# Optimization experiments

Hardware: AMD Instinct MI355X
Metric: run time of the kernel (lower is better)

## Reference

```python
import jax, jax.numpy as jnp
import numpy as np

BS = 16
CIN = 32          # input_channels
COUT = 64         # out_channels
OUT_DIM = 1024    # out_dim
S = 2
S0 = 1
K = S * (S0 + 1)  # non-overlapping patch size = 4
D = OUT_DIM * K   # input spatial length = 4096


def setup_inputs() -> dict:
    key = jax.random.key(0)
    k1, k2 = jax.random.split(key)
    x = jax.random.normal(k1, (BS, CIN, D), dtype=jnp.float32)
    # learned parameter, torch.randn init
    weight = jax.random.normal(k2, (COUT, CIN, D), dtype=jnp.float32)
    return {"x": x, "weight": weight}


def reference(x, weight):
    # sharing == 0 path of NonOverlappingLocallyConnected1d:
    #   out[b,o,p] = (1/sqrt(CIN)) * sum_{c,k} x[b,c,p*K+k] * weight[o,c,p*K+k]
    # Original materializes [bs,cout,cin,D] via broadcast multiply then sums
    # over (cin, K); fused here as a single einsum over non-overlapping patches.
    bs = x.shape[0]
    xr = x.reshape(bs, CIN, OUT_DIM, K)        # [b, c, p, k]
    wr = weight.reshape(COUT, CIN, OUT_DIM, K)  # [o, c, p, k]
    out = jnp.einsum('bcpk,ocpk->bop', xr, wr)  # [b, o, p]
    return out / jnp.sqrt(jnp.asarray(CIN, x.dtype))
```

## Files before the change

### kernel.cpp

```cpp
#include <hip/hip_runtime.h>

#define BS      16
#define CIN     32
#define COUT    64
#define OUT_DIM 1024
#define RS4     1024

__global__ __launch_bounds__(256, 6) void nolc1d_kernel(
    const float* __restrict__ x,
    const float* __restrict__ w,
    float* __restrict__ out)
{
    const int bid = blockIdx.x;
    const int xcd = bid & 7;
    const int j   = bid >> 3;
    const int og  = j & 15;
    const int bs  = (j >> 4) & 3;
    const int pg  = xcd + 8 * (j >> 6);
    const int o0  = og * 4;
    const int b0  = bs * 4;
    const int pf0 = pg * 32;

    const int t    = threadIdx.x;
    const int lane = t & 63;
    const int wv   = t >> 6;
    const int cs   = t >> 5;
    const int pp   = t & 31;

    const float4* __restrict__ x4 = (const float4*)x;
    const float4* __restrict__ w4 = (const float4*)w;

    float acc[4][4] = {};

    #pragma unroll 1
    for (int k = 0; k < 4; ++k) {
        const int c = cs + 8 * k;
        float4 xv[4];
        #pragma unroll
        for (int bi = 0; bi < 4; ++bi)
            xv[bi] = x4[((b0 + bi) * CIN + c) * RS4 + pf0 + pp];
        #pragma unroll
        for (int o = 0; o < 4; ++o) {
            const float4 wq = w4[((o0 + o) * CIN + c) * RS4 + pf0 + pp];
            #pragma unroll
            for (int bi = 0; bi < 4; ++bi)
                acc[bi][o] += xv[bi].x * wq.x + xv[bi].y * wq.y +
                              xv[bi].z * wq.z + xv[bi].w * wq.w;
        }
    }

    #pragma unroll
    for (int bi = 0; bi < 4; ++bi)
        #pragma unroll
        for (int o = 0; o < 4; ++o)
            acc[bi][o] += __shfl_xor(acc[bi][o], 32, 64);

    __shared__ float red[4][4][4][32];
    if (lane < 32) {
        #pragma unroll
        for (int bi = 0; bi < 4; ++bi)
            #pragma unroll
            for (int o = 0; o < 4; ++o)
                red[wv][bi][o][pp] = acc[bi][o];
    }
    __syncthreads();

    const float scale = 0.17677669529663687f;
    #pragma unroll
    for (int rep = 0; rep < 2; ++rep) {
        const int idx = t + 256 * rep;
        const int b   = idx >> 7;
        const int o   = (idx >> 5) & 3;
        const int p2  = idx & 31;
        const float s = red[0][b][o][p2] + red[1][b][o][p2] +
                        red[2][b][o][p2] + red[3][b][o][p2];
        out[((size_t)(b0 + b) * COUT + o0 + o) * OUT_DIM + pg * 32 + p2] =
            s * scale;
    }
}

extern "C" void kernel_launch(void* const* d_in, const int* in_sizes, int n_in,
                              void* d_out, int out_size, void* d_ws, size_t ws_size,
                              hipStream_t stream) {
    const float* x = (const float*)d_in[0];
    const float* w = (const float*)d_in[1];
    float* out = (float*)d_out;

    nolc1d_kernel<<<dim3(2048), dim3(256), 0, stream>>>(x, w, out);
}
```

Baseline: 87.12 us.

## Stage weight tile in LDS via direct global-to-LDS loads and cover all batches per block

Each block now handles all 16 batches for a 4-output, 32-patch tile, using 1024 threads instead of 256. The block's weight slice is loaded once into shared memory with global_load_lds, so weights are no longer refetched once per batch group across blocks. The cross-channel reduction reuses the same LDS buffer. In exchange, blocks are larger with 64KB LDS, the grid is smaller, and the weight load is not overlapped with compute, which may lower occupancy and latency hiding.

```diff
diff --git a/kernel.cpp b/kernel.cpp
--- a/kernel.cpp
+++ b/kernel.cpp
@@ -6,7 +6,7 @@
 #define OUT_DIM 1024
 #define RS4     1024
 
-__global__ __launch_bounds__(256, 6) void nolc1d_kernel(
+__global__ __launch_bounds__(1024, 8) void nolc1d_kernel(
     const float* __restrict__ x,
     const float* __restrict__ w,
     float* __restrict__ out)
@@ -15,37 +15,62 @@
     const int xcd = bid & 7;
     const int j   = bid >> 3;
     const int og  = j & 15;
-    const int bs  = (j >> 4) & 3;
-    const int pg  = xcd + 8 * (j >> 6);
+    const int pg  = xcd + 8 * (j >> 4);
     const int o0  = og * 4;
-    const int b0  = bs * 4;
     const int pf0 = pg * 32;
 
     const int t    = threadIdx.x;
     const int lane = t & 63;
     const int wv   = t >> 6;
-    const int cs   = t >> 5;
+    const int g    = t >> 8;
+    const int cs   = (t >> 5) & 7;
     const int pp   = t & 31;
+
+    __shared__ float4 ws[4096];
 
     const float4* __restrict__ x4 = (const float4*)x;
     const float4* __restrict__ w4 = (const float4*)w;
 
+    {
+        const int half = lane >> 5;
+        const int q    = lane & 31;
+        #pragma unroll
+        for (int i = 0; i < 4; ++i) {
+            const int s   = wv * 4 + i;
+            const int row = 2 * s + half;
+            const int cc  = row >> 2;
+            const int oo  = row & 3;
+            const float4* src =
+                &w4[((o0 + oo) * CIN + cc) * RS4 + pf0 + q];
+            float4* dst = &ws[s * 64];
+            __builtin_amdgcn_global_load_lds(
+                (const __attribute__((address_space(1))) void*)src,
+                (__attribute__((address_space(3))) void*)dst,
+                16, 0, 0);
+        }
+    }
+    __syncthreads();
+
     float acc[4][4] = {};
-
     #pragma unroll 1
     for (int k = 0; k < 4; ++k) {
-        const int c = cs + 8 * k;
-        float4 xv[4];
-        #pragma unroll
-        for (int bi = 0; bi < 4; ++bi)
-            xv[bi] = x4[((b0 + bi) * CIN + c) * RS4 + pf0 + pp];
+        const int c  = cs + 8 * k;
+        const int xo = c * RS4 + pf0 + pp;
+        const float4 xv0 = x4[(size_t)((4 * g + 0) * CIN) * RS4 + xo];
+        const float4 xv1 = x4[(size_t)((4 * g + 1) * CIN) * RS4 + xo];
+        const float4 xv2 = x4[(size_t)((4 * g + 2) * CIN) * RS4 + xo];
+        const float4 xv3 = x4[(size_t)((4 * g + 3) * CIN) * RS4 + xo];
         #pragma unroll
         for (int o = 0; o < 4; ++o) {
-            const float4 wq = w4[((o0 + o) * CIN + c) * RS4 + pf0 + pp];
-            #pragma unroll
-            for (int bi = 0; bi < 4; ++bi)
-                acc[bi][o] += xv[bi].x * wq.x + xv[bi].y * wq.y +
-                              xv[bi].z * wq.z + xv[bi].w * wq.w;
+            const float4 wq = ws[(c * 4 + o) * 32 + pp];
+            acc[0][o] += xv0.x * wq.x + xv0.y * wq.y +
+                         xv0.z * wq.z + xv0.w * wq.w;
+            acc[1][o] += xv1.x * wq.x + xv1.y * wq.y +
+                         xv1.z * wq.z + xv1.w * wq.w;
+            acc[2][o] += xv2.x * wq.x + xv2.y * wq.y +
+                         xv2.z * wq.z + xv2.w * wq.w;
+            acc[3][o] += xv3.x * wq.x + xv3.y * wq.y +
+                         xv3.z * wq.z + xv3.w * wq.w;
         }
     }
 
@@ -55,27 +80,34 @@
         for (int o = 0; o < 4; ++o)
             acc[bi][o] += __shfl_xor(acc[bi][o], 32, 64);
 
-    __shared__ float red[4][4][4][32];
+    __syncthreads();
+    const int csh = wv & 3;
     if (lane < 32) {
         #pragma unroll
-        for (int bi = 0; bi < 4; ++bi)
-            #pragma unroll
-            for (int o = 0; o < 4; ++o)
-                red[wv][bi][o][pp] = acc[bi][o];
+        for (int o = 0; o < 4; ++o)
+            ws[csh * 512 + (g * 4 + o) * 32 + pp] =
+                make_float4(acc[0][o], acc[1][o], acc[2][o], acc[3][o]);
     }
     __syncthreads();
 
     const float scale = 0.17677669529663687f;
-    #pragma unroll
-    for (int rep = 0; rep < 2; ++rep) {
-        const int idx = t + 256 * rep;
-        const int b   = idx >> 7;
-        const int o   = (idx >> 5) & 3;
-        const int p2  = idx & 31;
-        const float s = red[0][b][o][p2] + red[1][b][o][p2] +
-                        red[2][b][o][p2] + red[3][b][o][p2];
-        out[((size_t)(b0 + b) * COUT + o0 + o) * OUT_DIM + pg * 32 + p2] =
-            s * scale;
+    if (t < 512) {
+        const float4 a = ws[t];
+        const float4 b = ws[t + 512];
+        const float4 c = ws[t + 1024];
+        const float4 d = ws[t + 1536];
+        const int g2 = t >> 7;
+        const int oo = (t >> 5) & 3;
+        const int p2 = t & 31;
+        const size_t p = (size_t)pg * 32 + p2;
+        out[((size_t)(4 * g2 + 0) * COUT + o0 + oo) * OUT_DIM + p] =
+            (a.x + b.x + c.x + d.x) * scale;
+        out[((size_t)(4 * g2 + 1) * COUT + o0 + oo) * OUT_DIM + p] =
+            (a.y + b.y + c.y + d.y) * scale;
+        out[((size_t)(4 * g2 + 2) * COUT + o0 + oo) * OUT_DIM + p] =
+            (a.z + b.z + c.z + d.z) * scale;
+        out[((size_t)(4 * g2 + 3) * COUT + o0 + oo) * OUT_DIM + p] =
+            (a.w + b.w + c.w + d.w) * scale;
     }
 }
 
@@ -86,5 +118,5 @@
     const float* w = (const float*)d_in[1];
     float* out = (float*)d_out;
 
-    nolc1d_kernel<<<dim3(2048), dim3(256), 0, stream>>>(x, w, out);
+    nolc1d_kernel<<<dim3(512), dim3(1024), 0, stream>>>(x, w, out);
 }
```

Measured after the change: 87.74 us. No clear change (+0.7%).

## Stage full-batch x/w patch tiles in LDS via direct global-to-LDS loads

Applied to the files above, without the earlier changes.

Restructures blocking so each block covers all 16 batches, 16 output channels and 4 patches. The x and w tiles are loaded directly into LDS with global_load_lds, and the compute reads them from shared memory. This cuts redundant global reads of x and w across output and batch groups. In exchange it uses 64 KB of LDS per block, which limits occupancy, and it fetches shorter contiguous segments per row. The reduction now uses warp shuffles plus float4 output stores.

```diff
diff --git a/kernel.cpp b/kernel.cpp
--- a/kernel.cpp
+++ b/kernel.cpp
@@ -1,81 +1,107 @@
 #include <hip/hip_runtime.h>
 
-#define BS      16
 #define CIN     32
 #define COUT    64
 #define OUT_DIM 1024
 #define RS4     1024
 
-__global__ __launch_bounds__(256, 6) void nolc1d_kernel(
+__global__ __launch_bounds__(512, 4) void nolc1d_kernel(
     const float* __restrict__ x,
     const float* __restrict__ w,
     float* __restrict__ out)
 {
     const int bid = blockIdx.x;
     const int xcd = bid & 7;
-    const int j   = bid >> 3;
-    const int og  = j & 15;
-    const int bs  = (j >> 4) & 3;
-    const int pg  = xcd + 8 * (j >> 6);
-    const int o0  = og * 4;
-    const int b0  = bs * 4;
-    const int pf0 = pg * 32;
+    const int m   = bid >> 3;
+    const int og  = m & 3;
+    const int pgq = xcd * 32 + (m >> 2);
+    const int o0  = og * 16;
+    const int pf4 = pgq * 4;
 
     const int t    = threadIdx.x;
     const int lane = t & 63;
     const int wv   = t >> 6;
-    const int cs   = t >> 5;
-    const int pp   = t & 31;
+    const int cs   = t & 7;
+    const int p    = (t >> 3) & 3;
+    const int g    = (t >> 5) & 3;
+    const int oq   = t >> 7;
+
+    __shared__ float4 wls[2048];
+    __shared__ float4 xls[2048];
 
     const float4* __restrict__ x4 = (const float4*)x;
     const float4* __restrict__ w4 = (const float4*)w;
 
+    {
+        const int r = lane >> 2;
+        const int q = lane & 3;
+        #pragma unroll
+        for (int i = 0; i < 4; ++i) {
+            const int s  = wv * 4 + i;
+            const int rr = s * 16 + r;
+            const int hi = rr >> 5;
+            const int cc = rr & 31;
+            const float4* srcw =
+                &w4[((size_t)(o0 + hi) * CIN + cc) * RS4 + pf4 + q];
+            __builtin_amdgcn_global_load_lds(
+                (const __attribute__((address_space(1))) void*)srcw,
+                (__attribute__((address_space(3))) void*)&wls[s * 64],
+                16, 0, 0);
+            const float4* srcx =
+                &x4[((size_t)hi * CIN + cc) * RS4 + pf4 + q];
+            __builtin_amdgcn_global_load_lds(
+                (const __attribute__((address_space(1))) void*)srcx,
+                (__attribute__((address_space(3))) void*)&xls[s * 64],
+                16, 0, 0);
+        }
+    }
+    __syncthreads();
+
     float acc[4][4] = {};
-
-    #pragma unroll 1
-    for (int k = 0; k < 4; ++k) {
-        const int c = cs + 8 * k;
-        float4 xv[4];
+    #pragma unroll 2
+    for (int j = 0; j < 4; ++j) {
+        const int c = cs + 8 * j;
+        float4 xv[4], wq[4];
         #pragma unroll
         for (int bi = 0; bi < 4; ++bi)
-            xv[bi] = x4[((b0 + bi) * CIN + c) * RS4 + pf0 + pp];
+            xv[bi] = xls[((g * 4 + bi) * 32 + c) * 4 + p];
         #pragma unroll
-        for (int o = 0; o < 4; ++o) {
-            const float4 wq = w4[((o0 + o) * CIN + c) * RS4 + pf0 + pp];
+        for (int oi = 0; oi < 4; ++oi)
+            wq[oi] = wls[((oq * 4 + oi) * 32 + c) * 4 + p];
+        #pragma unroll
+        for (int bi = 0; bi < 4; ++bi)
             #pragma unroll
-            for (int bi = 0; bi < 4; ++bi)
-                acc[bi][o] += xv[bi].x * wq.x + xv[bi].y * wq.y +
-                              xv[bi].z * wq.z + xv[bi].w * wq.w;
-        }
+            for (int oi = 0; oi < 4; ++oi)
+                acc[bi][oi] += xv[bi].x * wq[oi].x + xv[bi].y * wq[oi].y +
+                               xv[bi].z * wq[oi].z + xv[bi].w * wq[oi].w;
     }
 
     #pragma unroll
-    for (int bi = 0; bi < 4; ++bi)
-        #pragma unroll
-        for (int o = 0; o < 4; ++o)
-            acc[bi][o] += __shfl_xor(acc[bi][o], 32, 64);
-
-    __shared__ float red[4][4][4][32];
-    if (lane < 32) {
+    for (int d = 1; d <= 4; d <<= 1)
         #pragma unroll
         for (int bi = 0; bi < 4; ++bi)
             #pragma unroll
-            for (int o = 0; o < 4; ++o)
-                red[wv][bi][o][pp] = acc[bi][o];
+            for (int oi = 0; oi < 4; ++oi)
+                acc[bi][oi] += __shfl_xor(acc[bi][oi], d, 64);
+
+    __syncthreads();
+    float* red = (float*)xls;
+    const float scale = 0.17677669529663687f;
+    if (cs == 0) {
+        #pragma unroll
+        for (int bi = 0; bi < 4; ++bi)
+            #pragma unroll
+            for (int oi = 0; oi < 4; ++oi)
+                red[((g * 4 + bi) * 16 + (oq * 4 + oi)) * 4 + p] =
+                    acc[bi][oi] * scale;
     }
     __syncthreads();
 
-    const float scale = 0.17677669529663687f;
-    #pragma unroll
-    for (int rep = 0; rep < 2; ++rep) {
-        const int idx = t + 256 * rep;
-        const int b   = idx >> 7;
-        const int o   = (idx >> 5) & 3;
-        const int p2  = idx & 31;
-        const float s = red[0][b][o][p2] + red[1][b][o][p2] +
-                        red[2][b][o][p2] + red[3][b][o][p2];
-        out[((size_t)(b0 + b) * COUT + o0 + o) * OUT_DIM + pg * 32 + p2] =
-            s * scale;
+    if (t < 256) {
+        const int b  = t >> 4;
+        const int ol = t & 15;
+        ((float4*)out)[((size_t)b * COUT + o0 + ol) * (OUT_DIM / 4) + pgq] =
+            ((float4*)red)[t];
     }
 }
 
@@ -86,5 +112,5 @@
     const float* w = (const float*)d_in[1];
     float* out = (float*)d_out;
 
-    nolc1d_kernel<<<dim3(2048), dim3(256), 0, stream>>>(x, w, out);
+    nolc1d_kernel<<<dim3(1024), dim3(512), 0, stream>>>(x, w, out);
 }
```

Measured after the change: 86.16 us. Within noise of the previous version (-1.1%).

## Stage x and weight tiles in LDS via async global_load_lds with double buffering

Applied to the files above, without the earlier changes.

Restructures the kernel so each 512-thread block covers all 16 batches, 4 output channels and 64 patches. It loops over channel pairs, double-buffering x and weight tiles into shared memory with global_load_lds direct-to-LDS loads. This lets each weight tile be reused across all batches in the block and overlaps the next channel's loads with the current compute. The cost is a much smaller grid (256 blocks), a large LDS footprint and a barrier every iteration, which may lower occupancy and latency hiding.

```diff
diff --git a/kernel.cpp b/kernel.cpp
--- a/kernel.cpp
+++ b/kernel.cpp
@@ -1,12 +1,11 @@
 #include <hip/hip_runtime.h>
 
-#define BS      16
 #define CIN     32
 #define COUT    64
 #define OUT_DIM 1024
 #define RS4     1024
 
-__global__ __launch_bounds__(256, 6) void nolc1d_kernel(
+__global__ __launch_bounds__(512, 2) void nolc1d_kernel(
     const float* __restrict__ x,
     const float* __restrict__ w,
     float* __restrict__ out)
@@ -15,67 +14,89 @@
     const int xcd = bid & 7;
     const int j   = bid >> 3;
     const int og  = j & 15;
-    const int bs  = (j >> 4) & 3;
-    const int pg  = xcd + 8 * (j >> 6);
+    const int pg  = xcd + 8 * (j >> 4);
     const int o0  = og * 4;
-    const int b0  = bs * 4;
-    const int pf0 = pg * 32;
+    const int pf0 = pg * 64;
 
     const int t    = threadIdx.x;
     const int lane = t & 63;
     const int wv   = t >> 6;
-    const int cs   = t >> 5;
-    const int pp   = t & 31;
+    const int q    = lane;
+    const int bq   = wv & 3;
+    const int cs   = wv >> 2;
+
+    __shared__ float4 wls[2][512];
+    __shared__ float4 xls[2][2048];
 
     const float4* __restrict__ x4 = (const float4*)x;
     const float4* __restrict__ w4 = (const float4*)w;
 
+    auto stage = [&](int buf, int ci) {
+        #pragma unroll
+        for (int i = 0; i < 5; ++i) {
+            const int r = wv * 5 + i;
+            if (r < 8) {
+                const float4* src =
+                    &w4[((size_t)(o0 + (r >> 1)) * CIN + 2 * ci + (r & 1))
+                        * RS4 + pf0 + q];
+                __builtin_amdgcn_global_load_lds(
+                    (const __attribute__((address_space(1))) void*)src,
+                    (__attribute__((address_space(3))) void*)&wls[buf][r * 64],
+                    16, 0, 0);
+            } else {
+                const int rr = r - 8;
+                const float4* src =
+                    &x4[((size_t)(rr >> 1) * CIN + 2 * ci + (rr & 1))
+                        * RS4 + pf0 + q];
+                __builtin_amdgcn_global_load_lds(
+                    (const __attribute__((address_space(1))) void*)src,
+                    (__attribute__((address_space(3))) void*)&xls[buf][rr * 64],
+                    16, 0, 0);
+            }
+        }
+    };
+
     float acc[4][4] = {};
 
+    stage(0, 0);
+    __syncthreads();
+
     #pragma unroll 1
-    for (int k = 0; k < 4; ++k) {
-        const int c = cs + 8 * k;
-        float4 xv[4];
+    for (int ci = 0; ci < 16; ++ci) {
+        if (ci < 15) stage((ci + 1) & 1, ci + 1);
+        const int buf = ci & 1;
+        float4 xv[4], wq[4];
         #pragma unroll
         for (int bi = 0; bi < 4; ++bi)
-            xv[bi] = x4[((b0 + bi) * CIN + c) * RS4 + pf0 + pp];
+            xv[bi] = xls[buf][((bq * 4 + bi) * 2 + cs) * 64 + q];
         #pragma unroll
-        for (int o = 0; o < 4; ++o) {
-            const float4 wq = w4[((o0 + o) * CIN + c) * RS4 + pf0 + pp];
+        for (int ol = 0; ol < 4; ++ol)
+            wq[ol] = wls[buf][(ol * 2 + cs) * 64 + q];
+        #pragma unroll
+        for (int bi = 0; bi < 4; ++bi)
             #pragma unroll
-            for (int bi = 0; bi < 4; ++bi)
-                acc[bi][o] += xv[bi].x * wq.x + xv[bi].y * wq.y +
-                              xv[bi].z * wq.z + xv[bi].w * wq.w;
-        }
+            for (int ol = 0; ol < 4; ++ol)
+                acc[bi][ol] += xv[bi].x * wq[ol].x + xv[bi].y * wq[ol].y +
+                               xv[bi].z * wq[ol].z + xv[bi].w * wq[ol].w;
+        if (ci < 15) __syncthreads();
     }
 
+    float* red = (float*)&xls[0][0];
     #pragma unroll
     for (int bi = 0; bi < 4; ++bi)
         #pragma unroll
-        for (int o = 0; o < 4; ++o)
-            acc[bi][o] += __shfl_xor(acc[bi][o], 32, 64);
-
-    __shared__ float red[4][4][4][32];
-    if (lane < 32) {
-        #pragma unroll
-        for (int bi = 0; bi < 4; ++bi)
-            #pragma unroll
-            for (int o = 0; o < 4; ++o)
-                red[wv][bi][o][pp] = acc[bi][o];
-    }
+        for (int ol = 0; ol < 4; ++ol)
+            red[(cs * 64 + (bq * 4 + bi) * 4 + ol) * 64 + q] = acc[bi][ol];
     __syncthreads();
 
     const float scale = 0.17677669529663687f;
+    const int cg = t >> 6;
     #pragma unroll
-    for (int rep = 0; rep < 2; ++rep) {
-        const int idx = t + 256 * rep;
-        const int b   = idx >> 7;
-        const int o   = (idx >> 5) & 3;
-        const int p2  = idx & 31;
-        const float s = red[0][b][o][p2] + red[1][b][o][p2] +
-                        red[2][b][o][p2] + red[3][b][o][p2];
-        out[((size_t)(b0 + b) * COUT + o0 + o) * OUT_DIM + pg * 32 + p2] =
-            s * scale;
+    for (int jj = 0; jj < 8; ++jj) {
+        const int combo = cg * 8 + jj;
+        const float s = red[combo * 64 + q] + red[(64 + combo) * 64 + q];
+        out[((size_t)(combo >> 2) * COUT + o0 + (combo & 3)) * OUT_DIM
+            + pf0 + q] = s * scale;
     }
 }
 
@@ -86,5 +107,5 @@
     const float* w = (const float*)d_in[1];
     float* out = (float*)d_out;
 
-    nolc1d_kernel<<<dim3(2048), dim3(256), 0, stream>>>(x, w, out);
+    nolc1d_kernel<<<dim3(256), dim3(512), 0, stream>>>(x, w, out);
 }
```

Result: slower. 91.39 us (+4.9%).
